# Kernel optimization log

Hardware: AMD Instinct MI355X
Metric: run time of the kernel (lower is better)

Reference implementation:

```python
import jax, jax.numpy as jnp
import numpy as np

B, T, HID = 2, 2048, 2048
NH, NKV = 16, 8
NOPE, ROPE = 128, 64
HD = NOPE + ROPE  # 192
VD = 128
KV_RANK, Q_RANK = 512, 1536
EPS = 1e-6
THETA = 10000.0
GROUPS = NH // NKV


def rmsnorm(x, w):
    var = jnp.mean(x * x, axis=-1, keepdims=True)
    return x * jax.lax.rsqrt(var + EPS) * w


def rope_cos_sin(seq_len, dtype):
    inv_freq = 1.0 / (THETA ** (jnp.arange(0, ROPE, 2, dtype=jnp.float32) / ROPE))
    t = jnp.arange(seq_len, dtype=jnp.float32)
    freqs = jnp.outer(t, inv_freq)
    emb = jnp.concatenate([freqs, freqs], axis=-1)  # [T, ROPE]
    return jnp.cos(emb).astype(dtype)[None, :, None, :], jnp.sin(emb).astype(dtype)[None, :, None, :]


def rotate_half(x):
    x1, x2 = x[..., : x.shape[-1] // 2], x[..., x.shape[-1] // 2 :]
    return jnp.concatenate([-x2, x1], axis=-1)


def setup_inputs() -> dict:
    key = jax.random.key(0)
    ks = jax.random.split(key, 7)
    s = 0.02
    return {
        "hidden_states": jax.random.normal(ks[0], (B, T, HID), jnp.float32),
        "q_a_w": jax.random.normal(ks[1], (HID, Q_RANK), jnp.float32) * s,
        "q_a_ln_w": jnp.ones((Q_RANK,), jnp.float32),
        "q_b_w": jax.random.normal(ks[2], (Q_RANK, NH * HD), jnp.float32) * s,
        "kv_a_w": jax.random.normal(ks[3], (HID, KV_RANK + NKV * ROPE), jnp.float32) * s,
        "kv_a_ln_w": jnp.ones((KV_RANK,), jnp.float32),
        "kv_b_w": jax.random.normal(ks[4], (KV_RANK, NKV * (NOPE + VD)), jnp.float32) * s,
        "o_w": jax.random.normal(ks[5], (NH * VD, HID), jnp.float32) * s,
    }


def reference(hidden_states, q_a_w, q_a_ln_w, q_b_w, kv_a_w, kv_a_ln_w, kv_b_w, o_w):
    x = hidden_states
    # Q low-rank path: a_proj -> RMSNorm -> b_proj
    q = rmsnorm(x @ q_a_w, q_a_ln_w) @ q_b_w
    q = q.reshape(B, T, NH, HD)
    q_nope, q_rope = q[..., :NOPE], q[..., NOPE:]
    # KV low-rank + decoupled rope key
    kv_raw = x @ kv_a_w
    kv_latent = rmsnorm(kv_raw[..., :KV_RANK], kv_a_ln_w)
    k_rope = kv_raw[..., KV_RANK:].reshape(B, T, NKV, ROPE)
    kv = (kv_latent @ kv_b_w).reshape(B, T, NKV, NOPE + VD)
    k_nope, v = kv[..., :NOPE], kv[..., NOPE:]
    # partial RoPE on rope slice only
    cos, sin = rope_cos_sin(T, x.dtype)
    q_rope = q_rope * cos + rotate_half(q_rope) * sin
    k_rope = k_rope * cos + rotate_half(k_rope) * sin
    q_full = jnp.concatenate([q_nope, q_rope], axis=-1)  # [B,T,NH,HD]
    k_full = jnp.concatenate([k_nope, k_rope], axis=-1)  # [B,T,NKV,HD]
    # GQA expansion (repeat_interleave over head dim)
    k_full = jnp.repeat(k_full, GROUPS, axis=2)  # [B,T,NH,HD]
    v_full = jnp.repeat(v, GROUPS, axis=2)       # [B,T,NH,VD]
    scale = HD ** -0.5
    scores = jnp.einsum("bqhd,bkhd->bhqk", q_full, k_full) * scale
    probs = jax.nn.softmax(scores, axis=-1)
    attn = jnp.einsum("bhqk,bkhd->bqhd", probs, v_full)
    out = attn.reshape(B, T, NH * VD) @ o_w
    return out
```

## Files before the change

kernel.cpp:

```cpp
#include <hip/hip_runtime.h>

using u16 = unsigned short;
using u32 = unsigned int;

typedef float f32x4 __attribute__((ext_vector_type(4)));
typedef __bf16 bf16x8 __attribute__((ext_vector_type(8)));

__device__ __forceinline__ u16 f2bf(float f){
  u32 u = __builtin_bit_cast(u32, f);
  u32 r = (u + 0x7fffu + ((u >> 16) & 1u)) >> 16;
  return (u16)r;
}
__device__ __forceinline__ float bf2f(u16 h){
  u32 u = ((u32)h) << 16;
  return __builtin_bit_cast(float, u);
}
__device__ __forceinline__ void gl2lds16(const void* g, void* l){
  __builtin_amdgcn_global_load_lds((const __attribute__((address_space(1))) u32*)g,
                                   (__attribute__((address_space(3))) u32*)l, 16, 0, 0);
}
__device__ __forceinline__ int swz24(int ck, int r){ return (ck & 24) | ((ck ^ r) & 7); }
__device__ __forceinline__ u32 cvtpk_bf16(float a, float b){
  u32 r; asm("v_cvt_pk_bf16_f32 %0, %1, %2" : "=v"(r) : "v"(a), "v"(b)); return r;
}
__device__ __forceinline__ float exp2_raw(float x){
  float r; asm("v_exp_f32 %0, %1" : "=v"(r) : "v"(x)); return r;
}

__global__ __launch_bounds__(256) void cvt_f32_bf16(const float* __restrict__ in,
                                                    u16* __restrict__ out, long n){
  long i = ((long)blockIdx.x*256 + threadIdx.x)*4;
  if (i >= n) return;
  float4 v = *(const float4*)(in + i);
  u16 o[4] = { f2bf(v.x), f2bf(v.y), f2bf(v.z), f2bf(v.w) };
  *(ushort4*)(out + i) = *(ushort4*)o;
}

__global__ __launch_bounds__(256) void transpose_w(const float* __restrict__ in,
                                                   u16* __restrict__ out, int K, int N){
  __shared__ float tile[32][33];
  int n0 = blockIdx.x*32, k0 = blockIdx.y*32;
  int tx = threadIdx.x, ty = threadIdx.y;
  for (int i = ty; i < 32; i += 8)
    tile[i][tx] = in[(size_t)(k0+i)*N + n0+tx];
  __syncthreads();
  for (int i = ty; i < 32; i += 8)
    out[(size_t)(n0+i)*K + k0+tx] = f2bf(tile[tx][i]);
}

__global__ __launch_bounds__(256) void rope_tables(float* __restrict__ cosT, float* __restrict__ sinT){
  int idx = blockIdx.x*256 + threadIdx.x;
  int t = idx >> 5, d = idx & 31;
  double inv = pow(10000.0, -(double)d / 32.0);
  double a = (double)t * inv;
  cosT[idx] = (float)cos(a);
  sinT[idx] = (float)sin(a);
}

__device__ __forceinline__ void remap_block(int NX, int& bx, int& by){
  int id = blockIdx.y*NX + blockIdx.x;
  bx = id >> 5;
  by = ((id & 7) << 2) | ((id >> 3) & 3);
}

template<int OUT_BF16>
__global__ __launch_bounds__(256) void gemm_bt(const u16* __restrict__ A,
                                               const u16* __restrict__ Bt,
                                               void* __restrict__ Cout,
                                               int M, int N, int K, float cscale){
  __shared__ u16 As[128*32];
  __shared__ u16 Bs[128*32];
  const int tid = threadIdx.x, lane = tid & 63, wave = tid >> 6;
  int bx, by; remap_block(gridDim.x, bx, by);
  const int m0 = by*128, n0 = bx*128;
  const int wm = (wave >> 1)*64, wn = (wave & 1)*64;
  const int g = lane >> 4, lr = lane & 15;
  f32x4 acc[4][4] = {};
  const int sr = (wave*2)*16 + (lane >> 2);
  const int sc = (lane & 3)*8;
  for (int k0 = 0; k0 < K; k0 += 32){
    __syncthreads();
    #pragma unroll
    for (int i = 0; i < 2; i++){
      int c = wave*2 + i;
      int r = sr + i*16;
      gl2lds16(A  + (size_t)(m0+r)*K + k0 + sc, (char*)As + c*1024);
      gl2lds16(Bt + (size_t)(n0+r)*K + k0 + sc, (char*)Bs + c*1024);
    }
    __syncthreads();
    bf16x8 af[4], bfr[4];
    #pragma unroll
    for (int mi = 0; mi < 4; mi++) af[mi]  = *reinterpret_cast<const bf16x8*>(&As[(wm+mi*16+lr)*32 + g*8]);
    #pragma unroll
    for (int ni = 0; ni < 4; ni++) bfr[ni] = *reinterpret_cast<const bf16x8*>(&Bs[(wn+ni*16+lr)*32 + g*8]);
    #pragma unroll
    for (int mi = 0; mi < 4; mi++)
      #pragma unroll
      for (int ni = 0; ni < 4; ni++)
        acc[mi][ni] = __builtin_amdgcn_mfma_f32_16x16x32_bf16(af[mi], bfr[ni], acc[mi][ni], 0,0,0);
  }
  #pragma unroll
  for (int mi = 0; mi < 4; mi++)
    #pragma unroll
    for (int ni = 0; ni < 4; ni++)
      #pragma unroll
      for (int r = 0; r < 4; r++){
        int row = m0 + wm + mi*16 + g*4 + r;
        int col = n0 + wn + ni*16 + lr;
        float v = acc[mi][ni][r];
        if (OUT_BF16) ((u16*)Cout)[(size_t)row*N + col] = f2bf(v*cscale);
        else          ((float*)Cout)[(size_t)row*N + col] = v;
      }
}

__global__ __launch_bounds__(256) void gemm_qb_rope(const u16* __restrict__ A,
                                                    const u16* __restrict__ Bt,
                                                    u16* __restrict__ C,
                                                    const float* __restrict__ cosT,
                                                    const float* __restrict__ sinT){
  constexpr int N = 3072, K = 1536;
  constexpr float qscale = 0.07216878364870322f * 1.44269504088896340f;
  __shared__ u16 As[128*32];
  __shared__ u16 Bs[128*32];
  const int tid = threadIdx.x, lane = tid & 63, wave = tid >> 6;
  int bx, by; remap_block(gridDim.x, bx, by);
  const int m0 = by*128, n0 = bx*128;
  const int wm = (wave >> 1)*64, wn = (wave & 1)*64;
  const int g = lane >> 4, lr = lane & 15;
  f32x4 acc[4][4] = {};
  const int sr = (wave*2)*16 + (lane >> 2);
  const int sc = (lane & 3)*8;
  for (int k0 = 0; k0 < K; k0 += 32){
    __syncthreads();
    #pragma unroll
    for (int i = 0; i < 2; i++){
      int c = wave*2 + i;
      int r = sr + i*16;
      gl2lds16(A  + (size_t)(m0+r)*K + k0 + sc, (char*)As + c*1024);
      gl2lds16(Bt + (size_t)(n0+r)*K + k0 + sc, (char*)Bs + c*1024);
    }
    __syncthreads();
    bf16x8 af[4], bfr[4];
    #pragma unroll
    for (int mi = 0; mi < 4; mi++) af[mi]  = *reinterpret_cast<const bf16x8*>(&As[(wm+mi*16+lr)*32 + g*8]);
    #pragma unroll
    for (int ni = 0; ni < 4; ni++) bfr[ni] = *reinterpret_cast<const bf16x8*>(&Bs[(wn+ni*16+lr)*32 + g*8]);
    #pragma unroll
    for (int mi = 0; mi < 4; mi++)
      #pragma unroll
      for (int ni = 0; ni < 4; ni++)
        acc[mi][ni] = __builtin_amdgcn_mfma_f32_16x16x32_bf16(af[mi], bfr[ni], acc[mi][ni], 0,0,0);
  }
  const bool rope = (((n0 + wn) >> 6) % 3) == 2;
  #pragma unroll
  for (int mi = 0; mi < 4; mi++)
    #pragma unroll
    for (int r = 0; r < 4; r++){
      int row = m0 + wm + mi*16 + g*4 + r;
      int t = row & 2047;
      u16* crow = C + (size_t)row*N + n0 + wn;
      if (rope){
        #pragma unroll
        for (int np = 0; np < 2; np++){
          int dp = np*16 + lr;
          float x1 = acc[mi][np][r]*qscale, x2 = acc[mi][np+2][r]*qscale;
          float cv = cosT[t*32 + dp], sv = sinT[t*32 + dp];
          crow[dp]      = f2bf(x1*cv - x2*sv);
          crow[dp + 32] = f2bf(x2*cv + x1*sv);
        }
      } else {
        #pragma unroll
        for (int ni = 0; ni < 4; ni++)
          crow[ni*16 + lr] = f2bf(acc[mi][ni][r]*qscale);
      }
    }
}

__global__ __launch_bounds__(256) void rmsnorm_bf16(const u16* __restrict__ in,
                                                    const float* __restrict__ w,
                                                    u16* __restrict__ out, int ncols, int instride){
  int row = blockIdx.x;
  const u16* x = in + (size_t)row*instride;
  int c = threadIdx.x;
  float xs[8];
  float ss = 0.f;
  int nch = ncols >> 3;
  if (c < nch){
    ushort4 a = *(const ushort4*)(x + c*8);
    ushort4 bq = *(const ushort4*)(x + c*8 + 4);
    u16 e[8] = {a.x,a.y,a.z,a.w,bq.x,bq.y,bq.z,bq.w};
    #pragma unroll
    for (int j = 0; j < 8; j++){ xs[j] = bf2f(e[j]); ss += xs[j]*xs[j]; }
  }
  #pragma unroll
  for (int m = 1; m < 64; m <<= 1) ss += __shfl_xor(ss, m, 64);
  __shared__ float p[4];
  if ((threadIdx.x & 63) == 0) p[threadIdx.x >> 6] = ss;
  __syncthreads();
  float inv = rsqrtf((p[0]+p[1]+p[2]+p[3]) / (float)ncols + 1e-6f);
  if (c < nch){
    u16 o[8];
    #pragma unroll
    for (int j = 0; j < 8; j++) o[j] = f2bf(xs[j]*inv*w[c*8+j]);
    *(ushort4*)(out + (size_t)row*ncols + c*8)     = *(ushort4*)o;
    *(ushort4*)(out + (size_t)row*ncols + c*8 + 4) = *(ushort4*)(o+4);
  }
}

__global__ __launch_bounds__(256) void kv_split_kernel(const u16* __restrict__ kvraw,
                                                       const float* __restrict__ lnw,
                                                       const float* __restrict__ cosT,
                                                       const float* __restrict__ sinT,
                                                       u16* __restrict__ kvlat,
                                                       u16* __restrict__ Kf){
  int row = blockIdx.x;
  int t = row & 2047, b = row >> 11;
  const u16* x = kvraw + (size_t)row*2560 + 1536;
  int c = threadIdx.x;
  float xs[4];
  float ss = 0.f;
  if (c < 128){
    ushort4 a = *(const ushort4*)(x + c*4);
    u16 e[4] = {a.x,a.y,a.z,a.w};
    #pragma unroll
    for (int j = 0; j < 4; j++){ xs[j] = bf2f(e[j]); ss += xs[j]*xs[j]; }
  }
  #pragma unroll
  for (int m = 1; m < 64; m <<= 1) ss += __shfl_xor(ss, m, 64);
  __shared__ float p[4];
  if ((threadIdx.x & 63) == 0) p[threadIdx.x >> 6] = ss;
  __syncthreads();
  float inv = rsqrtf((p[0]+p[1]+p[2]+p[3]) / 512.0f + 1e-6f);
  if (c < 128){
    u16 o[4];
    #pragma unroll
    for (int j = 0; j < 4; j++) o[j] = f2bf(xs[j]*inv*lnw[c*4+j]);
    *(ushort4*)(kvlat + (size_t)row*512 + c*4) = *(ushort4*)o;
  }
  int kh = threadIdx.x >> 5, dp = threadIdx.x & 31;
  float x1 = bf2f(x[512 + kh*64 + dp]), x2 = bf2f(x[512 + kh*64 + dp + 32]);
  float cv = cosT[t*32 + dp], sv = sinT[t*32 + dp];
  float o1 = x1*cv - x2*sv;
  float o2 = x2*cv + x1*sv;
  u16* kr = Kf + ((size_t)(b*8 + kh)*2048 + t)*192;
  int c1 = 128 + dp, c2 = 128 + dp + 32;
  kr[(swz24(c1 >> 3, t) << 3) | (c1 & 7)] = f2bf(o1);
  kr[(swz24(c2 >> 3, t) << 3) | (c2 & 7)] = f2bf(o2);
}

__global__ __launch_bounds__(256) void kv_rearrange(const u16* __restrict__ kv,
                                                    u16* __restrict__ vT,
                                                    u16* __restrict__ Kf){
  int bid = blockIdx.x;
  int tt = bid & 31, kvh = (bid >> 5) & 7, b = bid >> 8;
  int t0 = tt*64;
  __shared__ u16 tile[64][136];
  int tid = threadIdx.x;
  #pragma unroll
  for (int i = 0; i < 4; i++){
    int c2 = tid + i*256;
    int rr = c2 >> 4, ck = c2 & 15;
    int t = t0 + rr;
    int ck2 = (ck & 8) | ((ck ^ t) & 7);
    uint4 v = *(const uint4*)(kv + ((size_t)(b*2048 + t))*2048 + kvh*256 + ck*8);
    *(uint4*)(Kf + ((size_t)(b*8 + kvh)*2048 + t)*192 + ck2*8) = v;
  }
  #pragma unroll
  for (int i = 0; i < 4; i++){
    int c = tid + i*256;
    int r = c >> 4, ck = c & 15;
    const u16* src = kv + ((size_t)(b*2048 + t0 + r))*2048 + kvh*256 + 128 + ck*8;
    *(uint4*)&tile[r][ck*8] = *(const uint4*)src;
  }
  __syncthreads();
  #pragma unroll
  for (int i = 0; i < 4; i++){
    int c = tid + i*256;
    int vd = c >> 3, tc = c & 7;
    int stc = tc ^ (vd & 7);
    uint4 tv;
    u16* tp = (u16*)&tv;
    #pragma unroll
    for (int j = 0; j < 8; j++) tp[j] = tile[tc*8 + j][vd];
    *(uint4*)(vT + ((size_t)(b*8 + kvh)*128 + vd)*2048 + t0 + stc*8) = tv;
  }
}

__global__ __launch_bounds__(256, 2) void attn_kernel(const u16* __restrict__ Q,
                                                      const u16* __restrict__ Kf,
                                                      const u16* __restrict__ Vt,
                                                      u16* __restrict__ Oa){
  constexpr int T = 2048;
  constexpr int NT = T/64;
  __shared__ u16 Ks[64*192];
  __shared__ u16 Vs[2][128*64];
  __shared__ u16 Ps[4][2048];
  const int tid = threadIdx.x, lane = tid & 63, wave = tid >> 6;
  const int g = lane >> 4, lr = lane & 15;

  const int wg = blockIdx.x;
  const int role = (wg & 7)*64 + (wg >> 3);
  const int grp = role >> 5;
  const int b = grp >> 3, kvh = grp & 7;
  const int within = role & 31;
  const int h = kvh*2 + (within >> 4);
  const int q0 = (within & 15)*128 + wave*32;

  bf16x8 aq[2][6];
  #pragma unroll
  for (int qg = 0; qg < 2; qg++){
    const u16* qrow = Q + ((size_t)b*T + q0 + qg*16 + lr)*3072 + h*192;
    #pragma unroll
    for (int kc = 0; kc < 6; kc++)
      aq[qg][kc] = *reinterpret_cast<const bf16x8*>(qrow + kc*32 + g*8);
  }
  const u16* Kbase = Kf + (size_t)(b*8 + kvh)*T*192;
  const u16* Vbase = Vt + (size_t)(b*8 + kvh)*128*T;

  f32x4 ovb[2][8] = {};
  float mq[2] = {-1e30f, -1e30f};
  float lq[2] = {0.f, 0.f};

  auto stageK = [&](int kt){
    const u16* ksrc = Kbase + (size_t)kt*12288 + wave*3072 + lane*8;
    #pragma unroll
    for (int i = 0; i < 6; i++)
      gl2lds16(ksrc + i*512, (char*)Ks + (wave*6 + i)*1024);
  };
  auto stageV = [&](int kt, int buf){
    #pragma unroll
    for (int i = 0; i < 4; i++){
      int c = wave*4 + i;
      const u16* vsrc = Vbase + (size_t)(c*8 + (lane >> 3))*T + kt*64 + (lane & 7)*8;
      gl2lds16(vsrc, (char*)(&Vs[0][0]) + buf*16384 + c*1024);
    }
  };

  stageK(0);
  stageV(0, 0);
  __syncthreads();

  int buf = 0;
  for (int kt = 0; kt < NT; kt++){
    const bool notlast = (kt + 1 < NT);
    if (notlast) stageV(kt + 1, buf ^ 1);

    f32x4 s[2][4];
    __builtin_amdgcn_s_setprio(1);
    #pragma unroll
    for (int nb = 0; nb < 4; nb++){
      const int row = nb*16 + lr;
      f32x4 a0 = {0.f,0.f,0.f,0.f}, a1 = {0.f,0.f,0.f,0.f};
      #pragma unroll
      for (int kc = 0; kc < 6; kc++){
        int ckl = swz24(kc*4 + g, row);
        bf16x8 kf = *reinterpret_cast<const bf16x8*>(&Ks[row*192 + ckl*8]);
        a0 = __builtin_amdgcn_mfma_f32_16x16x32_bf16(kf, aq[0][kc], a0, 0,0,0);
        a1 = __builtin_amdgcn_mfma_f32_16x16x32_bf16(kf, aq[1][kc], a1, 0,0,0);
      }
      s[0][nb] = a0; s[1][nb] = a1;
    }
    __builtin_amdgcn_s_setprio(0);

    asm volatile("s_waitcnt lgkmcnt(0)" ::: "memory");
    __builtin_amdgcn_s_barrier();
    __builtin_amdgcn_sched_barrier(0);
    if (notlast) stageK(kt + 1);

    #pragma unroll
    for (int qg = 0; qg < 2; qg++){
      float pm = s[qg][0][0];
      #pragma unroll
      for (int nb = 0; nb < 4; nb++)
        #pragma unroll
        for (int r = 0; r < 4; r++)
          if (nb || r) pm = fmaxf(pm, s[qg][nb][r]);
      pm = fmaxf(pm, __shfl_xor(pm, 16, 64));
      pm = fmaxf(pm, __shfl_xor(pm, 32, 64));
      if (!__all(pm <= mq[qg] + 8.f)){
        float mn = fmaxf(mq[qg], pm);
        float corr = exp2_raw(mq[qg] - mn);
        mq[qg] = mn;
        lq[qg] *= corr;
        #pragma unroll
        for (int r = 0; r < 4; r++){
          float cr = __shfl(corr, (lane & 48) | (g*4 + r), 64);
          #pragma unroll
          for (int vb = 0; vb < 8; vb++) ovb[qg][vb][r] *= cr;
        }
      }
      float ls = 0.f;
      #pragma unroll
      for (int nb = 0; nb < 4; nb++){
        float e0 = exp2_raw(s[qg][nb][0] - mq[qg]);
        float e1 = exp2_raw(s[qg][nb][1] - mq[qg]);
        float e2 = exp2_raw(s[qg][nb][2] - mq[qg]);
        float e3 = exp2_raw(s[qg][nb][3] - mq[qg]);
        ls += (e0 + e1) + (e2 + e3);
        int stc = (2*nb + (g >> 1)) ^ (lr & 7);
        volatile u32* p = (volatile u32*)&Ps[wave][qg*1024 + lr*64 + stc*8 + (g & 1)*4];
        p[0] = cvtpk_bf16(e0, e1);
        p[1] = cvtpk_bf16(e2, e3);
      }
      lq[qg] += ls;
    }

    asm volatile("s_waitcnt lgkmcnt(0)" ::: "memory");
    __builtin_amdgcn_sched_barrier(0);

    bf16x8 ap[2][2];
    #pragma unroll
    for (int qg = 0; qg < 2; qg++)
      #pragma unroll
      for (int k2 = 0; k2 < 2; k2++){
        int ck = (k2*4 + g) ^ (lr & 7);
        ap[qg][k2] = *reinterpret_cast<const bf16x8*>(&Ps[wave][qg*1024 + lr*64 + ck*8]);
      }
    __builtin_amdgcn_s_setprio(1);
    #pragma unroll
    for (int vb = 0; vb < 8; vb++)
      #pragma unroll
      for (int k2 = 0; k2 < 2; k2++){
        int vd = vb*16 + lr;
        int ck = (k2*4 + g) ^ (vd & 7);
        bf16x8 bv = *reinterpret_cast<const bf16x8*>(&Vs[buf][vd*64 + ck*8]);
        ovb[0][vb] = __builtin_amdgcn_mfma_f32_16x16x32_bf16(ap[0][k2], bv, ovb[0][vb], 0,0,0);
        ovb[1][vb] = __builtin_amdgcn_mfma_f32_16x16x32_bf16(ap[1][k2], bv, ovb[1][vb], 0,0,0);
      }
    __builtin_amdgcn_s_setprio(0);

    if (notlast) __syncthreads();
    buf ^= 1;
  }

  #pragma unroll
  for (int qg = 0; qg < 2; qg++){
    float lt = lq[qg];
    lt += __shfl_xor(lt, 16, 64);
    lt += __shfl_xor(lt, 32, 64);
    float invq = 1.0f / lt;
    float inv_r[4];
    #pragma unroll
    for (int r = 0; r < 4; r++)
      inv_r[r] = __shfl(invq, (lane & 48) | (g*4 + r), 64);
    u16* obase = Oa + ((size_t)b*T + q0 + qg*16)*2048 + h*128;
    #pragma unroll
    for (int vb = 0; vb < 8; vb++)
      #pragma unroll
      for (int r = 0; r < 4; r++)
        obase[(size_t)(g*4 + r)*2048 + vb*16 + lr] = f2bf(ovb[qg][vb][r]*inv_r[r]);
  }
}

extern "C" void kernel_launch(void* const* d_in, const int* in_sizes, int n_in,
                              void* d_out, int out_size, void* d_ws, size_t ws_size,
                              hipStream_t stream){
  const float* hs      = (const float*)d_in[0];
  const float* q_a_w   = (const float*)d_in[1];
  const float* q_a_ln  = (const float*)d_in[2];
  const float* q_b_w   = (const float*)d_in[3];
  const float* kv_a_w  = (const float*)d_in[4];
  const float* kv_a_ln = (const float*)d_in[5];
  const float* kv_b_w  = (const float*)d_in[6];
  const float* o_w     = (const float*)d_in[7];

  char* ws = (char*)d_ws;
  size_t off = 0;
  auto alloc = [&](size_t bytes){ void* p = ws + off; off += bytes; return p; };
  u16*  Wqa   = (u16*)alloc(1536ull*2048*2);
  u16*  Wkva  = (u16*)alloc(1024ull*2048*2);
  u16*  Wqb   = (u16*)alloc(3072ull*1536*2);
  u16*  Wkvb  = (u16*)alloc(2048ull*512*2);
  u16*  Wo    = (u16*)alloc(2048ull*2048*2);
  u16*  XB    = (u16*)alloc(4096ull*2048*2);
  u16*  R23   = (u16*)alloc(4096ull*2560*2);
  u16*  QB    = (u16*)alloc(4096ull*3072*2);
  u16*  Qlat  = (u16*)alloc(4096ull*1536*2);
  u16*  KVlat = (u16*)alloc(4096ull*512*2);
  u16*  Kf    = (u16*)alloc(2ull*8*2048*192*2);
  u16*  Vt    = (u16*)alloc(2ull*8*128*2048*2);
  float* cosT = (float*)alloc(2048ull*32*4);
  float* sinT = (float*)alloc(2048ull*32*4);
  (void)ws_size; (void)in_sizes; (void)n_in; (void)out_size;

  u16* KVB = R23;

  cvt_f32_bf16<<<8192, 256, 0, stream>>>(hs, XB, 4096ll*2048);
  transpose_w<<<dim3(1536/32, 2048/32), dim3(32,8), 0, stream>>>(q_a_w,  Wqa,  2048, 1536);
  transpose_w<<<dim3(1024/32, 2048/32), dim3(32,8), 0, stream>>>(kv_a_w, Wkva, 2048, 1024);
  transpose_w<<<dim3(3072/32, 1536/32), dim3(32,8), 0, stream>>>(q_b_w,  Wqb,  1536, 3072);
  transpose_w<<<dim3(2048/32,  512/32), dim3(32,8), 0, stream>>>(kv_b_w, Wkvb,  512, 2048);
  transpose_w<<<dim3(2048/32, 2048/32), dim3(32,8), 0, stream>>>(o_w,    Wo,   2048, 2048);
  rope_tables<<<256, 256, 0, stream>>>(cosT, sinT);

  gemm_bt<1><<<dim3(20, 32), 256, 0, stream>>>(XB, Wqa, R23, 4096, 2560, 2048, 1.0f);
  rmsnorm_bf16<<<4096, 256, 0, stream>>>(R23, q_a_ln, Qlat, 1536, 2560);
  kv_split_kernel<<<4096, 256, 0, stream>>>(R23, kv_a_ln, cosT, sinT, KVlat, Kf);
  gemm_qb_rope<<<dim3(24, 32), 256, 0, stream>>>(Qlat, Wqb, QB, cosT, sinT);
  gemm_bt<1><<<dim3(16, 32), 256, 0, stream>>>(KVlat, Wkvb, KVB, 4096, 2048, 512, 1.0f);
  kv_rearrange<<<512, 256, 0, stream>>>(KVB, Vt, Kf);
  attn_kernel<<<512, 256, 0, stream>>>(QB, Kf, Vt, XB);
  gemm_bt<0><<<dim3(16, 32), 256, 0, stream>>>(XB, Wo, (float*)d_out, 4096, 2048, 2048, 1.0f);
}
```

Measured before the change: 346.5 us.

## Merge prep launches, fuse both RMSNorms, and batch Q-b and KV-b GEMMs

Folds the input conversion, five weight transposes and the rope table build into one grid-partitioned prep kernel. The two RMSNorm/split kernels are combined into a single per-row kernel that reads the R23 row once. The Q-b (with RoPE) and KV-b GEMMs run as one launch with block-id dispatch, so the smaller GEMM fills otherwise idle CUs. This cuts launch overhead and tail underutilisation, at the cost of branchy kernels and uneven per-block work in the combined GEMM.

```diff
diff --git a/kernel.cpp b/kernel.cpp
--- a/kernel.cpp
+++ b/kernel.cpp
@@ -27,20 +27,40 @@
   float r; asm("v_exp_f32 %0, %1" : "=v"(r) : "v"(x)); return r;
 }
 
-__global__ __launch_bounds__(256) void cvt_f32_bf16(const float* __restrict__ in,
-                                                    u16* __restrict__ out, long n){
-  long i = ((long)blockIdx.x*256 + threadIdx.x)*4;
-  if (i >= n) return;
-  float4 v = *(const float4*)(in + i);
-  u16 o[4] = { f2bf(v.x), f2bf(v.y), f2bf(v.z), f2bf(v.w) };
-  *(ushort4*)(out + i) = *(ushort4*)o;
-}
-
-__global__ __launch_bounds__(256) void transpose_w(const float* __restrict__ in,
-                                                   u16* __restrict__ out, int K, int N){
+__global__ __launch_bounds__(256) void prep_kernel(const float* __restrict__ hs, u16* __restrict__ XB,
+                                                   const float* __restrict__ q_a_w,  u16* __restrict__ Wqa,
+                                                   const float* __restrict__ kv_a_w, u16* __restrict__ Wkva,
+                                                   const float* __restrict__ q_b_w,  u16* __restrict__ Wqb,
+                                                   const float* __restrict__ kv_b_w, u16* __restrict__ Wkvb,
+                                                   const float* __restrict__ o_w,    u16* __restrict__ Wo,
+                                                   float* __restrict__ cosT, float* __restrict__ sinT){
   __shared__ float tile[32][33];
-  int n0 = blockIdx.x*32, k0 = blockIdx.y*32;
-  int tx = threadIdx.x, ty = threadIdx.y;
+  const int id = blockIdx.x;
+  if (id >= 15104){
+    long i = ((long)(id - 15104)*256 + threadIdx.x)*4;
+    float4 v = *(const float4*)(hs + i);
+    u16 o[4] = { f2bf(v.x), f2bf(v.y), f2bf(v.z), f2bf(v.w) };
+    *(ushort4*)(XB + i) = *(ushort4*)o;
+    return;
+  }
+  if (id >= 14848){
+    int idx = (id - 14848)*256 + threadIdx.x;
+    int t = idx >> 5, d = idx & 31;
+    double inv = pow(10000.0, -(double)d / 32.0);
+    double a = (double)t * inv;
+    cosT[idx] = (float)cos(a);
+    sinT[idx] = (float)sin(a);
+    return;
+  }
+  const float* in; u16* out; int K, N, lid;
+  if      (id <  3072){ in = q_a_w;  out = Wqa;  K = 2048; N = 1536; lid = id; }
+  else if (id <  5120){ in = kv_a_w; out = Wkva; K = 2048; N = 1024; lid = id - 3072; }
+  else if (id <  9728){ in = q_b_w;  out = Wqb;  K = 1536; N = 3072; lid = id - 5120; }
+  else if (id < 10752){ in = kv_b_w; out = Wkvb; K =  512; N = 2048; lid = id - 9728; }
+  else                { in = o_w;    out = Wo;   K = 2048; N = 2048; lid = id - 10752; }
+  const int tx = threadIdx.x & 31, ty = threadIdx.x >> 5;
+  const int nb = N >> 5;
+  const int n0 = (lid % nb)*32, k0 = (lid / nb)*32;
   for (int i = ty; i < 32; i += 8)
     tile[i][tx] = in[(size_t)(k0+i)*N + n0+tx];
   __syncthreads();
@@ -48,17 +68,7 @@
     out[(size_t)(n0+i)*K + k0+tx] = f2bf(tile[tx][i]);
 }
 
-__global__ __launch_bounds__(256) void rope_tables(float* __restrict__ cosT, float* __restrict__ sinT){
-  int idx = blockIdx.x*256 + threadIdx.x;
-  int t = idx >> 5, d = idx & 31;
-  double inv = pow(10000.0, -(double)d / 32.0);
-  double a = (double)t * inv;
-  cosT[idx] = (float)cos(a);
-  sinT[idx] = (float)sin(a);
-}
-
-__device__ __forceinline__ void remap_block(int NX, int& bx, int& by){
-  int id = blockIdx.y*NX + blockIdx.x;
+__device__ __forceinline__ void remap_id(int id, int& bx, int& by){
   bx = id >> 5;
   by = ((id & 7) << 2) | ((id >> 3) & 3);
 }
@@ -71,7 +81,7 @@
   __shared__ u16 As[128*32];
   __shared__ u16 Bs[128*32];
   const int tid = threadIdx.x, lane = tid & 63, wave = tid >> 6;
-  int bx, by; remap_block(gridDim.x, bx, by);
+  int bx, by; remap_id(blockIdx.y*gridDim.x + blockIdx.x, bx, by);
   const int m0 = by*128, n0 = bx*128;
   const int wm = (wave >> 1)*64, wn = (wave & 1)*64;
   const int g = lane >> 4, lr = lane & 15;
@@ -113,17 +123,23 @@
       }
 }
 
-__global__ __launch_bounds__(256) void gemm_qb_rope(const u16* __restrict__ A,
-                                                    const u16* __restrict__ Bt,
-                                                    u16* __restrict__ C,
-                                                    const float* __restrict__ cosT,
-                                                    const float* __restrict__ sinT){
-  constexpr int N = 3072, K = 1536;
+__global__ __launch_bounds__(256) void gemm_qb_kvb(const u16* __restrict__ Qlat,
+                                                   const u16* __restrict__ Wqb,
+                                                   u16* __restrict__ QB,
+                                                   const float* __restrict__ cosT,
+                                                   const float* __restrict__ sinT,
+                                                   const u16* __restrict__ KVlat,
+                                                   const u16* __restrict__ Wkvb,
+                                                   u16* __restrict__ KVB){
   constexpr float qscale = 0.07216878364870322f * 1.44269504088896340f;
   __shared__ u16 As[128*32];
   __shared__ u16 Bs[128*32];
+  const int id = blockIdx.x;
+  const u16 *A, *Bt; u16* C; int N, K; bool isqb;
+  int bx, by;
+  if (id < 768){ A = Qlat;  Bt = Wqb;  C = QB;  N = 3072; K = 1536; isqb = true;  remap_id(id, bx, by); }
+  else         { A = KVlat; Bt = Wkvb; C = KVB; N = 2048; K =  512; isqb = false; remap_id(id - 768, bx, by); }
   const int tid = threadIdx.x, lane = tid & 63, wave = tid >> 6;
-  int bx, by; remap_block(gridDim.x, bx, by);
   const int m0 = by*128, n0 = bx*128;
   const int wm = (wave >> 1)*64, wn = (wave & 1)*64;
   const int g = lane >> 4, lr = lane & 15;
@@ -151,94 +167,96 @@
       for (int ni = 0; ni < 4; ni++)
         acc[mi][ni] = __builtin_amdgcn_mfma_f32_16x16x32_bf16(af[mi], bfr[ni], acc[mi][ni], 0,0,0);
   }
-  const bool rope = (((n0 + wn) >> 6) % 3) == 2;
-  #pragma unroll
-  for (int mi = 0; mi < 4; mi++)
-    #pragma unroll
-    for (int r = 0; r < 4; r++){
-      int row = m0 + wm + mi*16 + g*4 + r;
-      int t = row & 2047;
-      u16* crow = C + (size_t)row*N + n0 + wn;
-      if (rope){
+  if (isqb){
+    const bool rope = (((n0 + wn) >> 6) % 3) == 2;
+    #pragma unroll
+    for (int mi = 0; mi < 4; mi++)
+      #pragma unroll
+      for (int r = 0; r < 4; r++){
+        int row = m0 + wm + mi*16 + g*4 + r;
+        int t = row & 2047;
+        u16* crow = C + (size_t)row*3072 + n0 + wn;
+        if (rope){
+          #pragma unroll
+          for (int np = 0; np < 2; np++){
+            int dp = np*16 + lr;
+            float x1 = acc[mi][np][r]*qscale, x2 = acc[mi][np+2][r]*qscale;
+            float cv = cosT[t*32 + dp], sv = sinT[t*32 + dp];
+            crow[dp]      = f2bf(x1*cv - x2*sv);
+            crow[dp + 32] = f2bf(x2*cv + x1*sv);
+          }
+        } else {
+          #pragma unroll
+          for (int ni = 0; ni < 4; ni++)
+            crow[ni*16 + lr] = f2bf(acc[mi][ni][r]*qscale);
+        }
+      }
+  } else {
+    #pragma unroll
+    for (int mi = 0; mi < 4; mi++)
+      #pragma unroll
+      for (int ni = 0; ni < 4; ni++)
         #pragma unroll
-        for (int np = 0; np < 2; np++){
-          int dp = np*16 + lr;
-          float x1 = acc[mi][np][r]*qscale, x2 = acc[mi][np+2][r]*qscale;
-          float cv = cosT[t*32 + dp], sv = sinT[t*32 + dp];
-          crow[dp]      = f2bf(x1*cv - x2*sv);
-          crow[dp + 32] = f2bf(x2*cv + x1*sv);
+        for (int r = 0; r < 4; r++){
+          int row = m0 + wm + mi*16 + g*4 + r;
+          int col = n0 + wn + ni*16 + lr;
+          C[(size_t)row*2048 + col] = f2bf(acc[mi][ni][r]);
         }
-      } else {
-        #pragma unroll
-        for (int ni = 0; ni < 4; ni++)
-          crow[ni*16 + lr] = f2bf(acc[mi][ni][r]*qscale);
-      }
-    }
-}
-
-__global__ __launch_bounds__(256) void rmsnorm_bf16(const u16* __restrict__ in,
-                                                    const float* __restrict__ w,
-                                                    u16* __restrict__ out, int ncols, int instride){
+  }
+}
+
+__global__ __launch_bounds__(256) void norm_split(const u16* __restrict__ R23,
+                                                  const float* __restrict__ q_ln,
+                                                  const float* __restrict__ kv_ln,
+                                                  const float* __restrict__ cosT,
+                                                  const float* __restrict__ sinT,
+                                                  u16* __restrict__ Qlat,
+                                                  u16* __restrict__ KVlat,
+                                                  u16* __restrict__ Kf){
   int row = blockIdx.x;
-  const u16* x = in + (size_t)row*instride;
+  int t = row & 2047, b = row >> 11;
+  const u16* x = R23 + (size_t)row*2560;
   int c = threadIdx.x;
-  float xs[8];
-  float ss = 0.f;
-  int nch = ncols >> 3;
-  if (c < nch){
+  float xq[8]; float ssq = 0.f;
+  if (c < 192){
     ushort4 a = *(const ushort4*)(x + c*8);
     ushort4 bq = *(const ushort4*)(x + c*8 + 4);
     u16 e[8] = {a.x,a.y,a.z,a.w,bq.x,bq.y,bq.z,bq.w};
     #pragma unroll
-    for (int j = 0; j < 8; j++){ xs[j] = bf2f(e[j]); ss += xs[j]*xs[j]; }
-  }
-  #pragma unroll
-  for (int m = 1; m < 64; m <<= 1) ss += __shfl_xor(ss, m, 64);
-  __shared__ float p[4];
-  if ((threadIdx.x & 63) == 0) p[threadIdx.x >> 6] = ss;
+    for (int j = 0; j < 8; j++){ xq[j] = bf2f(e[j]); ssq += xq[j]*xq[j]; }
+  }
+  float xk[4]; float ssk = 0.f;
+  if (c < 128){
+    ushort4 a = *(const ushort4*)(x + 1536 + c*4);
+    u16 e[4] = {a.x,a.y,a.z,a.w};
+    #pragma unroll
+    for (int j = 0; j < 4; j++){ xk[j] = bf2f(e[j]); ssk += xk[j]*xk[j]; }
+  }
+  #pragma unroll
+  for (int m = 1; m < 64; m <<= 1){
+    ssq += __shfl_xor(ssq, m, 64);
+    ssk += __shfl_xor(ssk, m, 64);
+  }
+  __shared__ float pq[4], pk[4];
+  if ((c & 63) == 0){ pq[c >> 6] = ssq; pk[c >> 6] = ssk; }
   __syncthreads();
-  float inv = rsqrtf((p[0]+p[1]+p[2]+p[3]) / (float)ncols + 1e-6f);
-  if (c < nch){
+  float invq = rsqrtf((pq[0]+pq[1]+pq[2]+pq[3]) / 1536.0f + 1e-6f);
+  float invk = rsqrtf((pk[0]+pk[1]+pk[2]+pk[3]) / 512.0f + 1e-6f);
+  if (c < 192){
     u16 o[8];
     #pragma unroll
-    for (int j = 0; j < 8; j++) o[j] = f2bf(xs[j]*inv*w[c*8+j]);
-    *(ushort4*)(out + (size_t)row*ncols + c*8)     = *(ushort4*)o;
-    *(ushort4*)(out + (size_t)row*ncols + c*8 + 4) = *(ushort4*)(o+4);
-  }
-}
-
-__global__ __launch_bounds__(256) void kv_split_kernel(const u16* __restrict__ kvraw,
-                                                       const float* __restrict__ lnw,
-                                                       const float* __restrict__ cosT,
-                                                       const float* __restrict__ sinT,
-                                                       u16* __restrict__ kvlat,
-                                                       u16* __restrict__ Kf){
-  int row = blockIdx.x;
-  int t = row & 2047, b = row >> 11;
-  const u16* x = kvraw + (size_t)row*2560 + 1536;
-  int c = threadIdx.x;
-  float xs[4];
-  float ss = 0.f;
-  if (c < 128){
-    ushort4 a = *(const ushort4*)(x + c*4);
-    u16 e[4] = {a.x,a.y,a.z,a.w};
-    #pragma unroll
-    for (int j = 0; j < 4; j++){ xs[j] = bf2f(e[j]); ss += xs[j]*xs[j]; }
-  }
-  #pragma unroll
-  for (int m = 1; m < 64; m <<= 1) ss += __shfl_xor(ss, m, 64);
-  __shared__ float p[4];
-  if ((threadIdx.x & 63) == 0) p[threadIdx.x >> 6] = ss;
-  __syncthreads();
-  float inv = rsqrtf((p[0]+p[1]+p[2]+p[3]) / 512.0f + 1e-6f);
+    for (int j = 0; j < 8; j++) o[j] = f2bf(xq[j]*invq*q_ln[c*8+j]);
+    *(ushort4*)(Qlat + (size_t)row*1536 + c*8)     = *(ushort4*)o;
+    *(ushort4*)(Qlat + (size_t)row*1536 + c*8 + 4) = *(ushort4*)(o+4);
+  }
   if (c < 128){
     u16 o[4];
     #pragma unroll
-    for (int j = 0; j < 4; j++) o[j] = f2bf(xs[j]*inv*lnw[c*4+j]);
-    *(ushort4*)(kvlat + (size_t)row*512 + c*4) = *(ushort4*)o;
-  }
-  int kh = threadIdx.x >> 5, dp = threadIdx.x & 31;
-  float x1 = bf2f(x[512 + kh*64 + dp]), x2 = bf2f(x[512 + kh*64 + dp + 32]);
+    for (int j = 0; j < 4; j++) o[j] = f2bf(xk[j]*invk*kv_ln[c*4+j]);
+    *(ushort4*)(KVlat + (size_t)row*512 + c*4) = *(ushort4*)o;
+  }
+  int kh = c >> 5, dp = c & 31;
+  float x1 = bf2f(x[2048 + kh*64 + dp]), x2 = bf2f(x[2048 + kh*64 + dp + 32]);
   float cv = cosT[t*32 + dp], sv = sinT[t*32 + dp];
   float o1 = x1*cv - x2*sv;
   float o2 = x2*cv + x1*sv;
@@ -485,19 +503,11 @@
 
   u16* KVB = R23;
 
-  cvt_f32_bf16<<<8192, 256, 0, stream>>>(hs, XB, 4096ll*2048);
-  transpose_w<<<dim3(1536/32, 2048/32), dim3(32,8), 0, stream>>>(q_a_w,  Wqa,  2048, 1536);
-  transpose_w<<<dim3(1024/32, 2048/32), dim3(32,8), 0, stream>>>(kv_a_w, Wkva, 2048, 1024);
-  transpose_w<<<dim3(3072/32, 1536/32), dim3(32,8), 0, stream>>>(q_b_w,  Wqb,  1536, 3072);
-  transpose_w<<<dim3(2048/32,  512/32), dim3(32,8), 0, stream>>>(kv_b_w, Wkvb,  512, 2048);
-  transpose_w<<<dim3(2048/32, 2048/32), dim3(32,8), 0, stream>>>(o_w,    Wo,   2048, 2048);
-  rope_tables<<<256, 256, 0, stream>>>(cosT, sinT);
-
+  prep_kernel<<<23296, 256, 0, stream>>>(hs, XB, q_a_w, Wqa, kv_a_w, Wkva,
+                                         q_b_w, Wqb, kv_b_w, Wkvb, o_w, Wo, cosT, sinT);
   gemm_bt<1><<<dim3(20, 32), 256, 0, stream>>>(XB, Wqa, R23, 4096, 2560, 2048, 1.0f);
-  rmsnorm_bf16<<<4096, 256, 0, stream>>>(R23, q_a_ln, Qlat, 1536, 2560);
-  kv_split_kernel<<<4096, 256, 0, stream>>>(R23, kv_a_ln, cosT, sinT, KVlat, Kf);
-  gemm_qb_rope<<<dim3(24, 32), 256, 0, stream>>>(Qlat, Wqb, QB, cosT, sinT);
-  gemm_bt<1><<<dim3(16, 32), 256, 0, stream>>>(KVlat, Wkvb, KVB, 4096, 2048, 512, 1.0f);
+  norm_split<<<4096, 256, 0, stream>>>(R23, q_a_ln, kv_a_ln, cosT, sinT, Qlat, KVlat, Kf);
+  gemm_qb_kvb<<<1280, 256, 0, stream>>>(Qlat, Wqb, QB, cosT, sinT, KVlat, Wkvb, KVB);
   kv_rearrange<<<512, 256, 0, stream>>>(KVB, Vt, Kf);
   attn_kernel<<<512, 256, 0, stream>>>(QB, Kf, Vt, XB);
   gemm_bt<0><<<dim3(16, 32), 256, 0, stream>>>(XB, Wo, (float*)d_out, 4096, 2048, 2048, 1.0f);
```

After: 348.0 us. About the same (+0.4%).
